# Performance work log

Hardware: AMD Instinct MI355X
Metric: run time of the kernel (lower is better)

The kernel has to match this reference:

```python
import jax, jax.numpy as jnp
import numpy as np

B, N, T_OBS, N_HEAD, D = 4, 2048, 8, 4, 16  # D = t_obs*2 = in/out feat of GAT
S, NSAMP = 2, 20
OUT_DIM = S * NSAMP  # 40
SEG = 64  # pedestrians per scene -> 32 scenes, block-diagonal mask


def _xavier(key, shape, gain=1.414):
    fan_in, fan_out = shape[-2], shape[-1]
    a = gain * np.sqrt(6.0 / (fan_in + fan_out))
    return jax.random.uniform(key, shape, jnp.float32, -a, a)


def setup_inputs() -> dict:
    key = jax.random.key(0)
    ks = jax.random.split(key, 12)
    x = jax.random.normal(ks[0], (B, N, T_OBS, 2), jnp.float32)
    # block-diagonal scene mask: 32 scenes of 64 peds each
    scene_id = jnp.arange(N) // SEG
    mask = (scene_id[:, None] == scene_id[None, :]).astype(jnp.float32)
    w = _xavier(ks[1], (N_HEAD, D, D))
    a_src = _xavier(ks[2], (N_HEAD, D, 1))
    a_dst = _xavier(ks[3], (N_HEAD, D, 1))
    bias = jnp.zeros((D,), jnp.float32)
    # MLP dims: (16,) + (16, 64) + (40,)
    W1 = _xavier(ks[4], (D, 16), gain=1.0)
    b1 = jnp.zeros((16,), jnp.float32)
    W2 = _xavier(ks[5], (16, 64), gain=1.0)
    b2 = jnp.zeros((64,), jnp.float32)
    W3 = _xavier(ks[6], (64, OUT_DIM), gain=1.0)
    b3 = jnp.zeros((OUT_DIM,), jnp.float32)
    return {"x": x, "mask": mask, "w": w, "a_src": a_src, "a_dst": a_dst,
            "bias": bias, "W1": W1, "b1": b1, "W2": W2, "b2": b2, "W3": W3, "b3": b3}


def reference(x, mask, w, a_src, a_dst, bias, W1, b1, W2, b2, W3, b3):
    b, n = x.shape[0], x.shape[1]
    node = x.reshape(b, n, -1)                       # (B, N, 16)
    # GAT
    hp = jnp.einsum('bni,hio->bhno', node, w)        # (B, H, N, D)
    attn_src = jnp.einsum('bhno,hoe->bhne', hp, a_src)[..., 0]  # (B, H, N)
    attn_dst = jnp.einsum('bhno,hoe->bhne', hp, a_dst)[..., 0]  # (B, H, N)
    attn = attn_src[:, :, :, None] * attn_dst[:, :, None, :]    # (B, H, N, N)
    attn = jnp.where(attn >= 0, attn, 0.2 * attn)    # leaky_relu(0.2)
    attn = jax.nn.softmax(attn, axis=-1)             # softmax over full row
    attn = attn * mask                                # mask AFTER softmax (as in source)
    out = jnp.einsum('bhnm,bhmo->bno', attn, hp) + bias
    out = out + hp.sum(axis=1)                        # skip connection
    # MLP head: activation applied BEFORE each Linear (per source), dropout disabled
    y = jax.nn.relu(out) @ W1 + b1
    y = jax.nn.relu(y) @ W2 + b2
    y = jax.nn.relu(y) @ W3 + b3
    y = y.reshape(b, n, NSAMP, -1)[..., 0:S]          # (B, N, 20, 2)
    return jnp.clip(jax.nn.sigmoid(y), 0.01, 0.99)
```

## Files before the change

kernel.cpp:

```cpp
#include <hip/hip_runtime.h>
#include <math.h>

#define L2E 1.4426950408889634f

#if defined(__has_builtin)
#if __has_builtin(__builtin_amdgcn_exp2f)
#define EXP2F(x) __builtin_amdgcn_exp2f(x)
#else
#define EXP2F(x) exp2f(x)
#endif
#else
#define EXP2F(x) exp2f(x)
#endif

__global__ __launch_bounds__(1024, 1) void k_fused(
    const float* __restrict__ x, const float* __restrict__ w,
    const float* __restrict__ a_src, const float* __restrict__ a_dst,
    const float* __restrict__ bias,
    const float* __restrict__ W1, const float* __restrict__ b1,
    const float* __restrict__ W2, const float* __restrict__ b2,
    const float* __restrict__ W3, const float* __restrict__ b3,
    float* __restrict__ out)
{
    __shared__ __align__(16) float RA[4 * 2048];
    __shared__ __align__(16) float RB[2048];
    __shared__ __align__(16) float RC[4096];
    __shared__ float cs_v[4][16], cd_v[4][16];
    __shared__ float s_v[4][32], me_v[4][32], den_v[4][32];
    __shared__ float dmx[16], dmn[16];
    __shared__ float feat[32][17];

    const int t = threadIdx.x;
    const int b = blockIdx.x >> 6;
    const int sc = (blockIdx.x >> 1) & 31;
    const int half = blockIdx.x & 1;
    const int n0 = sc * 64;
    const int r0 = n0 + half * 32;

    RB[1024 + t] = w[t];
    if (t < 256)
        ((float4*)RB)[t] = ((const float4*)(x + ((size_t)b * 2048 + n0) * 16))[t];
    if (t < 128) {
        int h = t >> 5, which = (t >> 4) & 1, i = t & 15;
        const float* av = which ? (a_dst + h * 16) : (a_src + h * 16);
        float acc = 0.f;
        #pragma unroll
        for (int o = 0; o < 16; ++o) acc = fmaf(w[h * 256 + i * 16 + o], av[o], acc);
        float* cv = which ? &cd_v[0][0] : &cs_v[0][0];
        cv[h * 16 + i] = acc;
    }
    __syncthreads();

    {
        const float4* xb = (const float4*)(x + (size_t)b * 2048 * 16);
        #pragma unroll
        for (int rep = 0; rep < 2; ++rep) {
            int n = t + rep * 1024;
            float4 x0 = xb[n * 4 + 0], x1 = xb[n * 4 + 1];
            float4 x2 = xb[n * 4 + 2], x3 = xb[n * 4 + 3];
            float xr[16] = {x0.x,x0.y,x0.z,x0.w, x1.x,x1.y,x1.z,x1.w,
                            x2.x,x2.y,x2.z,x2.w, x3.x,x3.y,x3.z,x3.w};
            #pragma unroll
            for (int h = 0; h < 4; ++h) {
                float acc = 0.f;
                #pragma unroll
                for (int i = 0; i < 16; ++i) acc = fmaf(xr[i], cd_v[h][i], acc);
                RA[h * 2048 + n] = acc;
            }
        }
    }
    if (t < 128) {
        int h = t >> 5, k = t & 31;
        float acc = 0.f;
        #pragma unroll
        for (int i = 0; i < 16; ++i)
            acc = fmaf(RB[(half * 32 + k) * 16 + i], cs_v[h][i], acc);
        s_v[h][k] = acc;
    }
    {
        int h = t >> 8, m = (t >> 2) & 63, oq = t & 3;
        float a0 = 0.f, a1 = 0.f, a2 = 0.f, a3 = 0.f;
        #pragma unroll
        for (int i = 0; i < 16; ++i) {
            float xv = RB[m * 16 + i];
            const float* wr = &RB[1024 + h * 256 + i * 16 + oq * 4];
            a0 = fmaf(xv, wr[0], a0);
            a1 = fmaf(xv, wr[1], a1);
            a2 = fmaf(xv, wr[2], a2);
            a3 = fmaf(xv, wr[3], a3);
        }
        ((float4*)RC)[(h * 64 + m) * 4 + oq] = make_float4(a0, a1, a2, a3);
    }
    __syncthreads();

    {
        int wv = t >> 6, L = t & 63;
        int h = wv >> 2, seg = wv & 3;
        const float4* d4 = (const float4*)RA;
        float4 v0 = d4[h * 512 + seg * 128 + L];
        float4 v1 = d4[h * 512 + seg * 128 + L + 64];
        float mx = fmaxf(fmaxf(fmaxf(v0.x, v0.y), fmaxf(v0.z, v0.w)),
                         fmaxf(fmaxf(v1.x, v1.y), fmaxf(v1.z, v1.w)));
        float mn = fminf(fminf(fminf(v0.x, v0.y), fminf(v0.z, v0.w)),
                         fminf(fminf(v1.x, v1.y), fminf(v1.z, v1.w)));
        #pragma unroll
        for (int off = 32; off >= 1; off >>= 1) {
            mx = fmaxf(mx, __shfl_xor(mx, off));
            mn = fminf(mn, __shfl_xor(mn, off));
        }
        if (L == 0) { dmx[wv] = mx; dmn[wv] = mn; }
    }
    __syncthreads();

    {
        int wv = t >> 6, L = t & 63;
        int h = wv >> 2, oct = wv & 3;
        float dmax = fmaxf(fmaxf(dmx[h*4], dmx[h*4+1]), fmaxf(dmx[h*4+2], dmx[h*4+3]));
        float dmin = fminf(fminf(dmn[h*4], dmn[h*4+1]), fminf(dmn[h*4+2], dmn[h*4+3]));
        float LPMAX = fmaxf(dmax, 0.2f * dmax);
        float LNMIN = fminf(dmin, 0.2f * dmin);
        const float4* d4 = (const float4*)(RA + h * 2048);
        float4 lpv[8], lnv[8];
        #pragma unroll
        for (int kk = 0; kk < 8; ++kk) {
            float4 dv = d4[L + 64 * kk];
            lpv[kk] = make_float4(fmaxf(dv.x, 0.2f*dv.x), fmaxf(dv.y, 0.2f*dv.y),
                                  fmaxf(dv.z, 0.2f*dv.z), fmaxf(dv.w, 0.2f*dv.w));
            lnv[kk] = make_float4(fminf(dv.x, 0.2f*dv.x), fminf(dv.y, 0.2f*dv.y),
                                  fminf(dv.z, 0.2f*dv.z), fminf(dv.w, 0.2f*dv.w));
        }
        for (int j = 0; j < 8; ++j) {
            int k = oct * 8 + j;
            float s = s_v[h][k];
            float sL = s * L2E;
            float me_nat = (s >= 0.f) ? s * LPMAX : s * LNMIN;
            float nme = -me_nat * L2E;
            float a0 = 0.f, a1 = 0.f, a2 = 0.f, a3 = 0.f;
            if (s >= 0.f) {
                #pragma unroll
                for (int kk = 0; kk < 8; ++kk) {
                    a0 += EXP2F(fmaf(sL, lpv[kk].x, nme));
                    a1 += EXP2F(fmaf(sL, lpv[kk].y, nme));
                    a2 += EXP2F(fmaf(sL, lpv[kk].z, nme));
                    a3 += EXP2F(fmaf(sL, lpv[kk].w, nme));
                }
            } else {
                #pragma unroll
                for (int kk = 0; kk < 8; ++kk) {
                    a0 += EXP2F(fmaf(sL, lnv[kk].x, nme));
                    a1 += EXP2F(fmaf(sL, lnv[kk].y, nme));
                    a2 += EXP2F(fmaf(sL, lnv[kk].z, nme));
                    a3 += EXP2F(fmaf(sL, lnv[kk].w, nme));
                }
            }
            float acc = (a0 + a1) + (a2 + a3);
            #pragma unroll
            for (int off = 32; off >= 1; off >>= 1) acc += __shfl_xor(acc, off);
            if (L == 0) { den_v[h][k] = acc; me_v[h][k] = nme; }
        }
    }
    __syncthreads();

    {
        int wv = t >> 6, L = t & 63;
        int h = wv >> 2, oct = wv & 3;
        int k = oct * 8 + (L >> 3), p = L & 7;
        float s = s_v[h][k];
        float sL = s * L2E, s2L = 0.2f * sL;
        float nme = me_v[h][k];
        float inv = 1.0f / den_v[h][k];
        float a[16];
        #pragma unroll
        for (int i = 0; i < 16; ++i) a[i] = 0.f;
        #pragma unroll
        for (int c = 0; c < 8; ++c) {
            int m = c * 8 + p;
            float d = RA[h * 2048 + n0 + m];
            float e = fmaxf(fmaf(sL, d, nme), fmaf(s2L, d, nme));
            float pr = EXP2F(e) * inv;
            const float4* hr = ((const float4*)RC) + (h * 64 + m) * 4;
            float4 h0 = hr[0], h1 = hr[1], h2 = hr[2], h3 = hr[3];
            a[0]  = fmaf(pr, h0.x, a[0]);  a[1]  = fmaf(pr, h0.y, a[1]);
            a[2]  = fmaf(pr, h0.z, a[2]);  a[3]  = fmaf(pr, h0.w, a[3]);
            a[4]  = fmaf(pr, h1.x, a[4]);  a[5]  = fmaf(pr, h1.y, a[5]);
            a[6]  = fmaf(pr, h1.z, a[6]);  a[7]  = fmaf(pr, h1.w, a[7]);
            a[8]  = fmaf(pr, h2.x, a[8]);  a[9]  = fmaf(pr, h2.y, a[9]);
            a[10] = fmaf(pr, h2.z, a[10]); a[11] = fmaf(pr, h2.w, a[11]);
            a[12] = fmaf(pr, h3.x, a[12]); a[13] = fmaf(pr, h3.y, a[13]);
            a[14] = fmaf(pr, h3.z, a[14]); a[15] = fmaf(pr, h3.w, a[15]);
        }
        #pragma unroll
        for (int i = 0; i < 16; ++i) {
            a[i] += __shfl_xor(a[i], 1);
            a[i] += __shfl_xor(a[i], 2);
            a[i] += __shfl_xor(a[i], 4);
        }
        if (p == 0) {
            float4* po4 = ((float4*)RB) + (h * 32 + k) * 4;
            po4[0] = make_float4(a[0],  a[1],  a[2],  a[3]);
            po4[1] = make_float4(a[4],  a[5],  a[6],  a[7]);
            po4[2] = make_float4(a[8],  a[9],  a[10], a[11]);
            po4[3] = make_float4(a[12], a[13], a[14], a[15]);
        }
    }
    __syncthreads();

    for (int u = t; u < 2560; u += 1024) RA[1360 + u] = W3[u];
    RA[272 + t] = W2[t];
    if (t < 256) RA[t] = W1[t];
    if (t < 16) RA[256 + t] = b1[t];
    else if (t >= 32 && t < 96) RA[1296 + (t - 32)] = b2[t - 32];
    else if (t >= 96 && t < 136) RA[3920 + (t - 96)] = b3[t - 96];
    if (t < 512) {
        int k = t >> 4, i = t & 15;
        float v = bias[i];
        #pragma unroll
        for (int h = 0; h < 4; ++h)
            v += RB[(h * 32 + k) * 16 + i] + RC[(h * 64 + half * 32 + k) * 16 + i];
        feat[k][i] = v;
    }
    __syncthreads();

    if (t < 512) {
        int k = t >> 4, j = t & 15;
        float acc = RA[256 + j];
        #pragma unroll
        for (int i = 0; i < 16; ++i)
            acc = fmaf(fmaxf(feat[k][i], 0.f), RA[i * 16 + j], acc);
        RC[k * 17 + j] = acc;
    }
    __syncthreads();

    {
        int k = t >> 5, g = t & 31;
        float acc0 = RA[1296 + g * 2], acc1 = RA[1296 + g * 2 + 1];
        #pragma unroll
        for (int j = 0; j < 16; ++j) {
            float r = fmaxf(RC[k * 17 + j], 0.f);
            acc0 = fmaf(r, RA[272 + j * 64 + g * 2], acc0);
            acc1 = fmaf(r, RA[272 + j * 64 + g * 2 + 1], acc1);
        }
        RC[544 + k * 65 + g * 2]     = acc0;
        RC[544 + k * 65 + g * 2 + 1] = acc1;
    }
    __syncthreads();

    for (int idx = t; idx < 1280; idx += 1024) {
        int k = idx / 40, c = idx % 40;
        float acc = RA[3920 + c];
        #pragma unroll 8
        for (int q = 0; q < 64; ++q)
            acc = fmaf(fmaxf(RC[544 + k * 65 + q], 0.f), RA[1360 + q * 40 + c], acc);
        float v = 1.0f / (1.0f + EXP2F(-acc * L2E));
        v = fminf(fmaxf(v, 0.01f), 0.99f);
        out[((size_t)(b * 2048) + r0 + k) * 40 + c] = v;
    }
}

extern "C" void kernel_launch(void* const* d_in, const int* in_sizes, int n_in,
                              void* d_out, int out_size, void* d_ws, size_t ws_size,
                              hipStream_t stream) {
    (void)in_sizes; (void)n_in; (void)out_size; (void)d_ws; (void)ws_size;
    const float* x     = (const float*)d_in[0];
    const float* w     = (const float*)d_in[2];
    const float* a_src = (const float*)d_in[3];
    const float* a_dst = (const float*)d_in[4];
    const float* bias  = (const float*)d_in[5];
    const float* W1    = (const float*)d_in[6];
    const float* b1    = (const float*)d_in[7];
    const float* W2    = (const float*)d_in[8];
    const float* b2    = (const float*)d_in[9];
    const float* W3    = (const float*)d_in[10];
    const float* b3    = (const float*)d_in[11];
    float* outp = (float*)d_out;

    hipLaunchKernelGGL(k_fused, dim3(256), dim3(1024), 0, stream,
                       x, w, a_src, a_dst, bias, W1, b1, W2, b2, W3, b3, outp);
}
```

Before: 35.23 us.

## Split each scene across four 512-thread blocks and restructure softmax denominator

The grid is doubled to 512 blocks of 512 threads, with each block handling 16 query rows instead of 32. The dst-score array now interleaves the four heads per node, and the x and hp tiles get padded strides. The softmax denominator pass changes from one shuffle reduction per row to each thread summing a 256-column chunk for one (head,row), followed by a cross-wave shared-memory sum. This aims to improve occupancy and cut shuffle traffic, at the cost of each block recomputing dst scores for all 2048 nodes, so that work is repeated more times overall.

```diff
diff --git a/kernel.cpp b/kernel.cpp
--- a/kernel.cpp
+++ b/kernel.cpp
@@ -13,7 +13,7 @@
 #define EXP2F(x) exp2f(x)
 #endif
 
-__global__ __launch_bounds__(1024, 1) void k_fused(
+__global__ __launch_bounds__(512, 4) void k_fused(
     const float* __restrict__ x, const float* __restrict__ w,
     const float* __restrict__ a_src, const float* __restrict__ a_dst,
     const float* __restrict__ bias,
@@ -22,24 +22,31 @@
     const float* __restrict__ W3, const float* __restrict__ b3,
     float* __restrict__ out)
 {
-    __shared__ __align__(16) float RA[4 * 2048];
-    __shared__ __align__(16) float RB[2048];
-    __shared__ __align__(16) float RC[4096];
+    __shared__ __align__(16) float RA[8192];
+    __shared__ __align__(16) float RB[2112];
+    __shared__ __align__(16) float RC[5120];
     __shared__ float cs_v[4][16], cd_v[4][16];
-    __shared__ float s_v[4][32], me_v[4][32], den_v[4][32];
-    __shared__ float dmx[16], dmn[16];
-    __shared__ float feat[32][17];
+    __shared__ float s_v[64];
+    __shared__ float me_v[64], den_v[64];
+    __shared__ float mxs[8][4], mns[8][4];
+    __shared__ float pden[8 * 64];
+    __shared__ float feat[16][17];
 
     const int t = threadIdx.x;
-    const int b = blockIdx.x >> 6;
-    const int sc = (blockIdx.x >> 1) & 31;
-    const int half = blockIdx.x & 1;
+    const int b  = blockIdx.x >> 7;
+    const int sc = (blockIdx.x >> 2) & 31;
+    const int qt = blockIdx.x & 3;
     const int n0 = sc * 64;
-    const int r0 = n0 + half * 32;
-
-    RB[1024 + t] = w[t];
-    if (t < 256)
-        ((float4*)RB)[t] = ((const float4*)(x + ((size_t)b * 2048 + n0) * 16))[t];
+    const int r0 = n0 + qt * 16;
+
+    {
+        const float* xb = x + ((size_t)b * 2048 + n0) * 16;
+        int u0 = t, u1 = t + 512;
+        RB[(u0 >> 4) * 17 + (u0 & 15)] = xb[u0];
+        RB[(u1 >> 4) * 17 + (u1 & 15)] = xb[u1];
+    }
+    RB[1088 + t] = w[t];
+    RB[1600 + t] = w[512 + t];
     if (t < 128) {
         int h = t >> 5, which = (t >> 4) & 1, i = t & 15;
         const float* av = which ? (a_dst + h * 16) : (a_src + h * 16);
@@ -54,131 +61,140 @@
     {
         const float4* xb = (const float4*)(x + (size_t)b * 2048 * 16);
         #pragma unroll
-        for (int rep = 0; rep < 2; ++rep) {
-            int n = t + rep * 1024;
+        for (int rep = 0; rep < 4; ++rep) {
+            int n = t + rep * 512;
             float4 x0 = xb[n * 4 + 0], x1 = xb[n * 4 + 1];
             float4 x2 = xb[n * 4 + 2], x3 = xb[n * 4 + 3];
             float xr[16] = {x0.x,x0.y,x0.z,x0.w, x1.x,x1.y,x1.z,x1.w,
                             x2.x,x2.y,x2.z,x2.w, x3.x,x3.y,x3.z,x3.w};
+            float dh[4];
             #pragma unroll
             for (int h = 0; h < 4; ++h) {
                 float acc = 0.f;
                 #pragma unroll
                 for (int i = 0; i < 16; ++i) acc = fmaf(xr[i], cd_v[h][i], acc);
-                RA[h * 2048 + n] = acc;
+                dh[h] = acc;
             }
-        }
-    }
-    if (t < 128) {
-        int h = t >> 5, k = t & 31;
+            ((float4*)RA)[n] = make_float4(dh[0], dh[1], dh[2], dh[3]);
+        }
+    }
+    if (t < 64) {
+        int h = t >> 4, k = t & 15;
         float acc = 0.f;
         #pragma unroll
         for (int i = 0; i < 16; ++i)
-            acc = fmaf(RB[(half * 32 + k) * 16 + i], cs_v[h][i], acc);
-        s_v[h][k] = acc;
-    }
-    {
-        int h = t >> 8, m = (t >> 2) & 63, oq = t & 3;
+            acc = fmaf(RB[(qt * 16 + k) * 17 + i], cs_v[h][i], acc);
+        s_v[h * 16 + k] = acc;
+    }
+    #pragma unroll
+    for (int rep = 0; rep < 2; ++rep) {
+        int u = t + rep * 512;
+        int h = u >> 8, m = (u >> 2) & 63, oq = u & 3;
         float a0 = 0.f, a1 = 0.f, a2 = 0.f, a3 = 0.f;
         #pragma unroll
         for (int i = 0; i < 16; ++i) {
-            float xv = RB[m * 16 + i];
-            const float* wr = &RB[1024 + h * 256 + i * 16 + oq * 4];
+            float xv = RB[m * 17 + i];
+            const float* wr = &RB[1088 + h * 256 + i * 16 + oq * 4];
             a0 = fmaf(xv, wr[0], a0);
             a1 = fmaf(xv, wr[1], a1);
             a2 = fmaf(xv, wr[2], a2);
             a3 = fmaf(xv, wr[3], a3);
         }
-        ((float4*)RC)[(h * 64 + m) * 4 + oq] = make_float4(a0, a1, a2, a3);
+        ((float4*)RC)[(h * 64 + m) * 5 + oq] = make_float4(a0, a1, a2, a3);
+    }
+    __syncthreads();
+
+    {
+        const float4* d4 = (const float4*)RA;
+        float4 v0 = d4[t * 4 + 0], v1 = d4[t * 4 + 1];
+        float4 v2 = d4[t * 4 + 2], v3 = d4[t * 4 + 3];
+        float mx0 = fmaxf(fmaxf(v0.x, v1.x), fmaxf(v2.x, v3.x));
+        float mx1 = fmaxf(fmaxf(v0.y, v1.y), fmaxf(v2.y, v3.y));
+        float mx2 = fmaxf(fmaxf(v0.z, v1.z), fmaxf(v2.z, v3.z));
+        float mx3 = fmaxf(fmaxf(v0.w, v1.w), fmaxf(v2.w, v3.w));
+        float mn0 = fminf(fminf(v0.x, v1.x), fminf(v2.x, v3.x));
+        float mn1 = fminf(fminf(v0.y, v1.y), fminf(v2.y, v3.y));
+        float mn2 = fminf(fminf(v0.z, v1.z), fminf(v2.z, v3.z));
+        float mn3 = fminf(fminf(v0.w, v1.w), fminf(v2.w, v3.w));
+        #pragma unroll
+        for (int off = 32; off >= 1; off >>= 1) {
+            mx0 = fmaxf(mx0, __shfl_xor(mx0, off));
+            mx1 = fmaxf(mx1, __shfl_xor(mx1, off));
+            mx2 = fmaxf(mx2, __shfl_xor(mx2, off));
+            mx3 = fmaxf(mx3, __shfl_xor(mx3, off));
+            mn0 = fminf(mn0, __shfl_xor(mn0, off));
+            mn1 = fminf(mn1, __shfl_xor(mn1, off));
+            mn2 = fminf(mn2, __shfl_xor(mn2, off));
+            mn3 = fminf(mn3, __shfl_xor(mn3, off));
+        }
+        if ((t & 63) == 0) {
+            int wv = t >> 6;
+            mxs[wv][0] = mx0; mxs[wv][1] = mx1; mxs[wv][2] = mx2; mxs[wv][3] = mx3;
+            mns[wv][0] = mn0; mns[wv][1] = mn1; mns[wv][2] = mn2; mns[wv][3] = mn3;
+        }
     }
     __syncthreads();
 
     {
         int wv = t >> 6, L = t & 63;
-        int h = wv >> 2, seg = wv & 3;
-        const float4* d4 = (const float4*)RA;
-        float4 v0 = d4[h * 512 + seg * 128 + L];
-        float4 v1 = d4[h * 512 + seg * 128 + L + 64];
-        float mx = fmaxf(fmaxf(fmaxf(v0.x, v0.y), fmaxf(v0.z, v0.w)),
-                         fmaxf(fmaxf(v1.x, v1.y), fmaxf(v1.z, v1.w)));
-        float mn = fminf(fminf(fminf(v0.x, v0.y), fminf(v0.z, v0.w)),
-                         fminf(fminf(v1.x, v1.y), fminf(v1.z, v1.w)));
-        #pragma unroll
-        for (int off = 32; off >= 1; off >>= 1) {
-            mx = fmaxf(mx, __shfl_xor(mx, off));
-            mn = fminf(mn, __shfl_xor(mn, off));
-        }
-        if (L == 0) { dmx[wv] = mx; dmn[wv] = mn; }
+        int h = L >> 4;
+        float dmax = mxs[0][h], dmin = mns[0][h];
+        #pragma unroll
+        for (int wq = 1; wq < 8; ++wq) {
+            dmax = fmaxf(dmax, mxs[wq][h]);
+            dmin = fminf(dmin, mns[wq][h]);
+        }
+        float LP = fmaxf(dmax, 0.2f * dmax);
+        float LN = fminf(dmin, 0.2f * dmin);
+        float s  = s_v[L];
+        float me_nat = (s >= 0.f) ? s * LP : s * LN;
+        float nme = -me_nat * L2E;
+        float sL = s * L2E, s2L = 0.2f * sL;
+        if (wv == 0) me_v[L] = nme;
+        const float* dcol = RA + wv * 1024 + h;
+        float a0 = 0.f, a1 = 0.f, a2 = 0.f, a3 = 0.f;
+        #pragma unroll 4
+        for (int c = 0; c < 256; c += 4) {
+            float d0 = dcol[(c + 0) * 4];
+            float d1 = dcol[(c + 1) * 4];
+            float d2 = dcol[(c + 2) * 4];
+            float d3 = dcol[(c + 3) * 4];
+            a0 += EXP2F(fmaxf(fmaf(sL, d0, nme), fmaf(s2L, d0, nme)));
+            a1 += EXP2F(fmaxf(fmaf(sL, d1, nme), fmaf(s2L, d1, nme)));
+            a2 += EXP2F(fmaxf(fmaf(sL, d2, nme), fmaf(s2L, d2, nme)));
+            a3 += EXP2F(fmaxf(fmaf(sL, d3, nme), fmaf(s2L, d3, nme)));
+        }
+        pden[wv * 64 + L] = (a0 + a1) + (a2 + a3);
+    }
+    __syncthreads();
+    if (t < 64) {
+        float s = 0.f;
+        #pragma unroll
+        for (int wq = 0; wq < 8; ++wq) s += pden[wq * 64 + t];
+        den_v[t] = s;
     }
     __syncthreads();
 
     {
         int wv = t >> 6, L = t & 63;
-        int h = wv >> 2, oct = wv & 3;
-        float dmax = fmaxf(fmaxf(dmx[h*4], dmx[h*4+1]), fmaxf(dmx[h*4+2], dmx[h*4+3]));
-        float dmin = fminf(fminf(dmn[h*4], dmn[h*4+1]), fminf(dmn[h*4+2], dmn[h*4+3]));
-        float LPMAX = fmaxf(dmax, 0.2f * dmax);
-        float LNMIN = fminf(dmin, 0.2f * dmin);
-        const float4* d4 = (const float4*)(RA + h * 2048);
-        float4 lpv[8], lnv[8];
-        #pragma unroll
-        for (int kk = 0; kk < 8; ++kk) {
-            float4 dv = d4[L + 64 * kk];
-            lpv[kk] = make_float4(fmaxf(dv.x, 0.2f*dv.x), fmaxf(dv.y, 0.2f*dv.y),
-                                  fmaxf(dv.z, 0.2f*dv.z), fmaxf(dv.w, 0.2f*dv.w));
-            lnv[kk] = make_float4(fminf(dv.x, 0.2f*dv.x), fminf(dv.y, 0.2f*dv.y),
-                                  fminf(dv.z, 0.2f*dv.z), fminf(dv.w, 0.2f*dv.w));
-        }
-        for (int j = 0; j < 8; ++j) {
-            int k = oct * 8 + j;
-            float s = s_v[h][k];
-            float sL = s * L2E;
-            float me_nat = (s >= 0.f) ? s * LPMAX : s * LNMIN;
-            float nme = -me_nat * L2E;
-            float a0 = 0.f, a1 = 0.f, a2 = 0.f, a3 = 0.f;
-            if (s >= 0.f) {
-                #pragma unroll
-                for (int kk = 0; kk < 8; ++kk) {
-                    a0 += EXP2F(fmaf(sL, lpv[kk].x, nme));
-                    a1 += EXP2F(fmaf(sL, lpv[kk].y, nme));
-                    a2 += EXP2F(fmaf(sL, lpv[kk].z, nme));
-                    a3 += EXP2F(fmaf(sL, lpv[kk].w, nme));
-                }
-            } else {
-                #pragma unroll
-                for (int kk = 0; kk < 8; ++kk) {
-                    a0 += EXP2F(fmaf(sL, lnv[kk].x, nme));
-                    a1 += EXP2F(fmaf(sL, lnv[kk].y, nme));
-                    a2 += EXP2F(fmaf(sL, lnv[kk].z, nme));
-                    a3 += EXP2F(fmaf(sL, lnv[kk].w, nme));
-                }
-            }
-            float acc = (a0 + a1) + (a2 + a3);
-            #pragma unroll
-            for (int off = 32; off >= 1; off >>= 1) acc += __shfl_xor(acc, off);
-            if (L == 0) { den_v[h][k] = acc; me_v[h][k] = nme; }
-        }
-    }
-    __syncthreads();
-
-    {
-        int wv = t >> 6, L = t & 63;
-        int h = wv >> 2, oct = wv & 3;
-        int k = oct * 8 + (L >> 3), p = L & 7;
-        float s = s_v[h][k];
+        int h = wv >> 1;
+        int kk = (wv & 1) * 8 + (L >> 3);
+        int p = L & 7;
+        int row = h * 16 + kk;
+        float s = s_v[row];
         float sL = s * L2E, s2L = 0.2f * sL;
-        float nme = me_v[h][k];
-        float inv = 1.0f / den_v[h][k];
+        float nme = me_v[row];
+        float inv = 1.0f / den_v[row];
         float a[16];
         #pragma unroll
         for (int i = 0; i < 16; ++i) a[i] = 0.f;
         #pragma unroll
         for (int c = 0; c < 8; ++c) {
             int m = c * 8 + p;
-            float d = RA[h * 2048 + n0 + m];
+            float d = RA[(n0 + m) * 4 + h];
             float e = fmaxf(fmaf(sL, d, nme), fmaf(s2L, d, nme));
             float pr = EXP2F(e) * inv;
-            const float4* hr = ((const float4*)RC) + (h * 64 + m) * 4;
+            const float4* hr = ((const float4*)RC) + (h * 64 + m) * 5;
             float4 h0 = hr[0], h1 = hr[1], h2 = hr[2], h3 = hr[3];
             a[0]  = fmaf(pr, h0.x, a[0]);  a[1]  = fmaf(pr, h0.y, a[1]);
             a[2]  = fmaf(pr, h0.z, a[2]);  a[3]  = fmaf(pr, h0.w, a[3]);
@@ -196,32 +212,32 @@
             a[i] += __shfl_xor(a[i], 4);
         }
         if (p == 0) {
-            float4* po4 = ((float4*)RB) + (h * 32 + k) * 4;
-            po4[0] = make_float4(a[0],  a[1],  a[2],  a[3]);
-            po4[1] = make_float4(a[4],  a[5],  a[6],  a[7]);
-            po4[2] = make_float4(a[8],  a[9],  a[10], a[11]);
-            po4[3] = make_float4(a[12], a[13], a[14], a[15]);
-        }
-    }
-    __syncthreads();
-
-    for (int u = t; u < 2560; u += 1024) RA[1360 + u] = W3[u];
+            float* po = &RB[(h * 16 + kk) * 16];
+            #pragma unroll
+            for (int i = 0; i < 16; ++i) po[i] = a[i];
+        }
+    }
+    __syncthreads();
+
+    #pragma unroll
+    for (int rep = 0; rep < 5; ++rep) RA[1360 + t + rep * 512] = W3[t + rep * 512];
     RA[272 + t] = W2[t];
+    RA[784 + t] = W2[512 + t];
     if (t < 256) RA[t] = W1[t];
     if (t < 16) RA[256 + t] = b1[t];
     else if (t >= 32 && t < 96) RA[1296 + (t - 32)] = b2[t - 32];
     else if (t >= 96 && t < 136) RA[3920 + (t - 96)] = b3[t - 96];
-    if (t < 512) {
+    if (t < 256) {
         int k = t >> 4, i = t & 15;
         float v = bias[i];
         #pragma unroll
         for (int h = 0; h < 4; ++h)
-            v += RB[(h * 32 + k) * 16 + i] + RC[(h * 64 + half * 32 + k) * 16 + i];
+            v += RB[(h * 16 + k) * 16 + i] + RC[(h * 64 + qt * 16 + k) * 20 + i];
         feat[k][i] = v;
     }
     __syncthreads();
 
-    if (t < 512) {
+    if (t < 256) {
         int k = t >> 4, j = t & 15;
         float acc = RA[256 + j];
         #pragma unroll
@@ -245,7 +261,7 @@
     }
     __syncthreads();
 
-    for (int idx = t; idx < 1280; idx += 1024) {
+    for (int idx = t; idx < 640; idx += 512) {
         int k = idx / 40, c = idx % 40;
         float acc = RA[3920 + c];
         #pragma unroll 8
@@ -274,6 +290,6 @@
     const float* b3    = (const float*)d_in[11];
     float* outp = (float*)d_out;
 
-    hipLaunchKernelGGL(k_fused, dim3(256), dim3(1024), 0, stream,
+    hipLaunchKernelGGL(k_fused, dim3(512), dim3(512), 0, stream,
                        x, w, a_src, a_dst, bias, W1, b1, W2, b2, W3, b3, outp);
 }
```

Result: no change. 35.54 us (+0.9%).
